# Optimization experiments

Measured on AMD Instinct MI355X. Metric: run time of the kernel, lower is better.

Reference implementation:

```python
import jax, jax.numpy as jnp
import numpy as np
import math

B, D, H, N, L = 32, 64, 8, 4096, 12
DK = D // H  # 8
APT = 10

def conv1x1_relu(x, w, b):
    # x: [B, C, N, L]; w: [O, C]; b: [O]  (1x1 conv == channel matmul)
    return jax.nn.relu(jnp.einsum('oc,bcnl->bonl', w, x) + b[None, :, None, None])

def setup_inputs() -> dict:
    key = jax.random.key(0)
    ks = jax.random.split(key, 12)
    s = 1.0 / math.sqrt(D)
    return {
        'x': jax.random.normal(ks[0], (B, D, N, L), jnp.float32),
        'wq': jax.random.normal(ks[1], (D, D), jnp.float32) * s,
        'bq': jnp.zeros((D,), jnp.float32),
        'wv': jax.random.normal(ks[2], (D, D), jnp.float32) * s,
        'bv': jnp.zeros((D,), jnp.float32),
        'wc': jax.random.normal(ks[3], (D, D), jnp.float32) * s,
        'bc': jnp.zeros((D,), jnp.float32),
        'memory': jax.random.normal(ks[4], (H, L, N, DK), jnp.float32) * 0.02,
        'weight': jnp.ones((D, N, L), jnp.float32),
        'bias': jnp.zeros((D, N, L), jnp.float32),
        'nv1': jax.random.normal(ks[5], (N, APT), jnp.float32),
        'nv2': jax.random.normal(ks[6], (APT, N), jnp.float32),
    }

def reference(x, wq, bq, wv, bv, wc, bc, memory, weight, bias, nv1, nv2):
    scale = 1.0 / math.sqrt(DK)
    q = conv1x1_relu(x, wq, bq)               # [B, D, N, L]
    v = conv1x1_relu(x, wv, bv)               # [B, D, N, L]
    # [B, D, N, L] -> [B, H, dk, N, L] -> [B, H, L, N, dk]
    v5 = jnp.transpose(v.reshape(B, H, DK, N, L), (0, 1, 4, 3, 2))
    q5 = jnp.transpose(q.reshape(B, H, DK, N, L), (0, 1, 4, 3, 2))
    key_sm = jax.nn.softmax(memory * scale, axis=-1)       # [H, L, N, dk]
    q_sm = jax.nn.softmax(q5 * scale, axis=-1)             # [B, H, L, N, dk]
    Aapt = jax.nn.softmax(jax.nn.relu(nv1 @ nv2), axis=-1) # [N, N]
    kv = jnp.einsum('hlnx,bhlny->bhlxy', key_sm, v5)       # [B,H,L,dk,dk]
    attn_qkv = jnp.einsum('bhlnx,bhlxy->bhlny', q_sm, kv)  # [B,H,L,N,dk]
    # 'nm,bhlnc->bhlnc' sums Aapt over m -> row-sum scaling of value
    row = jnp.sum(Aapt, axis=1)                            # [N]
    attn_dyn = row[None, None, None, :, None] * v5
    y = attn_qkv + attn_dyn                                # [B,H,L,N,dk]
    y = jnp.transpose(y, (0, 1, 4, 3, 2)).reshape(B, D, N, L)
    y = conv1x1_relu(y, wc, bc)
    out = y * weight[None] + bias[None] + y
    return out
```

## Files before the change

kernel.cpp:

```cpp
#include <hip/hip_runtime.h>
#include <math.h>
#include <stdint.h>

#define BB 32
#define DD 64
#define HH 8
#define NNN 4096
#define LL 12
#define PP (NNN * LL)

#define NTILES_A 24
#define CHUNK_A (64 * NTILES_A)
#define NCHUNK_A (PP / CHUNK_A)

#define NTILES_B 12
#define CHUNK_B (64 * NTILES_B)
#define NCHUNK_B (PP / CHUNK_B)

#define VSTRIDE 68
#define SCALE 0.35355339059327373f

typedef const __attribute__((address_space(1))) uint32_t gu32;
typedef __attribute__((address_space(3))) uint32_t lu32;

__device__ __forceinline__ void dma16(const float* src, float* dst) {
    __builtin_amdgcn_global_load_lds((gu32*)src, (lu32*)dst, 16, 0, 0);
}

__device__ __forceinline__ int xsw(int p, int c4) {
    return (p << 6) + (((c4 ^ (p & 7)) & 15) << 2);
}

__global__ void prep(const float* __restrict__ wq, const float* __restrict__ wv,
                     const float* __restrict__ wc, float* __restrict__ wt)
{
    const int i = blockIdx.x * 256 + threadIdx.x;
    const int o = i >> 6, c = i & 63;
    wt[c * 64 + o]        = wq[i];
    wt[4096 + c * 64 + o] = wv[i];
    wt[8192 + c * 64 + o] = wc[i];
}

__global__ void prep_ksm(const float* __restrict__ mem, float* __restrict__ ksm)
{
    const int g = blockIdx.x * 256 + threadIdx.x;
    const int p = g >> 3, h = g & 7;
    const int n = p / 12, l = p - n * 12;
    const float4* mp = (const float4*)(mem + (((size_t)(h * 12 + l) * NNN + n) << 3));
    float4 a0 = mp[0], a1 = mp[1];
    float v0 = a0.x * SCALE, v1 = a0.y * SCALE, v2 = a0.z * SCALE, v3 = a0.w * SCALE;
    float v4 = a1.x * SCALE, v5 = a1.y * SCALE, v6 = a1.z * SCALE, v7 = a1.w * SCALE;
    float m = fmaxf(fmaxf(fmaxf(v0, v1), fmaxf(v2, v3)),
                    fmaxf(fmaxf(v4, v5), fmaxf(v6, v7)));
    float e0 = __expf(v0 - m), e1 = __expf(v1 - m), e2 = __expf(v2 - m), e3 = __expf(v3 - m);
    float e4 = __expf(v4 - m), e5 = __expf(v5 - m), e6 = __expf(v6 - m), e7 = __expf(v7 - m);
    float inv = 1.0f / (e0 + e1 + e2 + e3 + e4 + e5 + e6 + e7);
    float4* op = (float4*)(ksm + ((size_t)g << 3));
    op[0] = make_float4(e0 * inv, e1 * inv, e2 * inv, e3 * inv);
    op[1] = make_float4(e4 * inv, e5 * inv, e6 * inv, e7 * inv);
}

__global__ void prep_wb(const float* __restrict__ wgt, const float* __restrict__ bsa,
                        float* __restrict__ wb)
{
    const size_t i = (size_t)blockIdx.x * 256 + threadIdx.x;
    wb[i * 2]     = wgt[i] + 1.0f;
    wb[i * 2 + 1] = bsa[i];
}

__global__ __launch_bounds__(512, 2)
void pass_a(const float* __restrict__ x, const float* __restrict__ wvt,
            const float* __restrict__ bv, const float* __restrict__ mem,
            const float* __restrict__ ksm,
            float* __restrict__ kv)
{
    __shared__ float xb0[64 * 64];
    __shared__ float xb1[64 * 64];
    __shared__ float ksl[64 * 64];
    __shared__ float v_tile[64 * VSTRIDE];

    const int t = threadIdx.x;
    const int b = blockIdx.y;
    const int chunk0 = blockIdx.x * CHUNK_A;

    const int p1 = t & 63;
    const int og = t >> 6;
    const int o0 = og << 3;
    const int o0u = __builtin_amdgcn_readfirstlane(o0);
    const float* __restrict__ wvu = wvt + o0u;

    float bvl[8];
#pragma unroll
    for (int j = 0; j < 8; j++) bvl[j] = bv[o0 + j];

    const int wid = t >> 6;
    const int ln  = t & 63;
    const int g_r = ln >> 4;
    const int g_c4 = (ln & 15) << 2;

    const int h2 = (t >> 3) & 7;
    const int x2 = t & 7;
    const int l0 = t >> 6;
    const int l1 = 8 + (t >> 6);
    const bool has2 = (t < 256);

    float acc[2][8];
#pragma unroll
    for (int q = 0; q < 2; q++)
#pragma unroll
        for (int y = 0; y < 8; y++) acc[q][y] = 0.f;

    const float* xb = x + (size_t)(b * 64) * PP;

    auto issue_x = [&](float* dst, int pn) {
        const int r0 = wid << 3;
        dma16(xb + (size_t)(r0 + g_r) * PP + pn + g_c4, dst + (r0 << 6));
        dma16(xb + (size_t)(r0 + 4 + g_r) * PP + pn + g_c4, dst + ((r0 + 4) << 6));
    };
    auto issue_ks = [&](int pn) {
        const int fo = wid << 9;
        const float* s0 = ksm + (((size_t)pn) << 6) + fo + (ln << 2);
        dma16(s0, ksl + fo);
        dma16(s0 + 256, ksl + fo + 256);
    };
    auto fallback_ks = [&](int pbase) {
        int pos = t >> 3, h = t & 7;
        int pg = pbase + pos;
        int n = pg / 12;
        int l = pg - n * 12;
        const float4* mp = (const float4*)(mem + (((size_t)(h * 12 + l) * NNN + n) << 3));
        float4 a0 = mp[0], a1 = mp[1];
        float v0 = a0.x * SCALE, v1 = a0.y * SCALE, v2 = a0.z * SCALE, v3 = a0.w * SCALE;
        float v4 = a1.x * SCALE, v5 = a1.y * SCALE, v6 = a1.z * SCALE, v7 = a1.w * SCALE;
        float m = fmaxf(fmaxf(fmaxf(v0, v1), fmaxf(v2, v3)),
                        fmaxf(fmaxf(v4, v5), fmaxf(v6, v7)));
        float e0 = __expf(v0 - m), e1 = __expf(v1 - m), e2 = __expf(v2 - m), e3 = __expf(v3 - m);
        float e4 = __expf(v4 - m), e5 = __expf(v5 - m), e6 = __expf(v6 - m), e7 = __expf(v7 - m);
        float inv = 1.0f / (e0 + e1 + e2 + e3 + e4 + e5 + e6 + e7);
        float4* kp = (float4*)(ksl + (pos << 6) + (h << 3));
        kp[0] = make_float4(e0 * inv, e1 * inv, e2 * inv, e3 * inv);
        kp[1] = make_float4(e4 * inv, e5 * inv, e6 * inv, e7 * inv);
    };

    issue_x(xb0, chunk0);
    if (ksm) issue_ks(chunk0); else fallback_ks(chunk0);
    __syncthreads();

    for (int tile = 0; tile < NTILES_A; tile++) {
        const int pbase = chunk0 + tile * 64;
        float* bufA = (tile & 1) ? xb1 : xb0;
        float* bufB = (tile & 1) ? xb0 : xb1;
        const bool more = (tile + 1) < NTILES_A;

        if (more) issue_x(bufB, pbase + 64);

        float va[8];
#pragma unroll
        for (int j = 0; j < 8; j++) va[j] = 0.f;
        for (int c = 0; c < 64; c += 4) {
            float xs0 = bufA[(c << 6) + p1];
            float xs1 = bufA[((c + 1) << 6) + p1];
            float xs2 = bufA[((c + 2) << 6) + p1];
            float xs3 = bufA[((c + 3) << 6) + p1];
            const float* w0 = wvu + c * 64;
#pragma unroll
            for (int j = 0; j < 8; j++) {
                va[j] += w0[j] * xs0;
                va[j] += w0[64 + j] * xs1;
                va[j] += w0[128 + j] * xs2;
                va[j] += w0[192 + j] * xs3;
            }
        }
        {
            const int slot = ((og ^ (p1 >> 3)) & 7) << 3;
            float4* vt4 = (float4*)(v_tile + p1 * VSTRIDE + slot);
            float4 w;
            w.x = fmaxf(va[0] + bvl[0], 0.f);
            w.y = fmaxf(va[1] + bvl[1], 0.f);
            w.z = fmaxf(va[2] + bvl[2], 0.f);
            w.w = fmaxf(va[3] + bvl[3], 0.f);
            vt4[0] = w;
            w.x = fmaxf(va[4] + bvl[4], 0.f);
            w.y = fmaxf(va[5] + bvl[5], 0.f);
            w.z = fmaxf(va[6] + bvl[6], 0.f);
            w.w = fmaxf(va[7] + bvl[7], 0.f);
            vt4[1] = w;
        }
        __syncthreads();

        const int r = pbase % 12;
        {
            int s = l0 - r;
            if (s < 0) s += 12;
            for (int p = s; p < 64; p += 12) {
                float ksv = ksl[(p << 6) + (h2 << 3) + x2];
                const int slot = ((h2 ^ (p >> 3)) & 7) << 3;
                const float4* vp = (const float4*)(v_tile + p * VSTRIDE + slot);
                float4 u0 = vp[0], u1 = vp[1];
                acc[0][0] += ksv * u0.x; acc[0][1] += ksv * u0.y;
                acc[0][2] += ksv * u0.z; acc[0][3] += ksv * u0.w;
                acc[0][4] += ksv * u1.x; acc[0][5] += ksv * u1.y;
                acc[0][6] += ksv * u1.z; acc[0][7] += ksv * u1.w;
            }
        }
        if (has2) {
            int s = l1 - r;
            if (s < 0) s += 12;
            for (int p = s; p < 64; p += 12) {
                float ksv = ksl[(p << 6) + (h2 << 3) + x2];
                const int slot = ((h2 ^ (p >> 3)) & 7) << 3;
                const float4* vp = (const float4*)(v_tile + p * VSTRIDE + slot);
                float4 u0 = vp[0], u1 = vp[1];
                acc[1][0] += ksv * u0.x; acc[1][1] += ksv * u0.y;
                acc[1][2] += ksv * u0.z; acc[1][3] += ksv * u0.w;
                acc[1][4] += ksv * u1.x; acc[1][5] += ksv * u1.y;
                acc[1][6] += ksv * u1.z; acc[1][7] += ksv * u1.w;
            }
        }
        __syncthreads();

        if (more) { if (ksm) issue_ks(pbase + 64); else fallback_ks(pbase + 64); }
    }

    {
        float* kvp = kv + (((size_t)((b * 12 + l0) * 8 + h2)) << 6) + (x2 << 3);
#pragma unroll
        for (int y = 0; y < 8; y++) atomicAdd(kvp + y, acc[0][y]);
    }
    if (has2) {
        float* kvp = kv + (((size_t)((b * 12 + l1) * 8 + h2)) << 6) + (x2 << 3);
#pragma unroll
        for (int y = 0; y < 8; y++) atomicAdd(kvp + y, acc[1][y]);
    }
}

__global__ __launch_bounds__(256, 2)
void pass_b(const float* __restrict__ x, const float* __restrict__ wqt,
            const float* __restrict__ wvt, const float* __restrict__ wct,
            const float* __restrict__ bq, const float* __restrict__ bv,
            const float* __restrict__ bc, const float* __restrict__ kv,
            const float* __restrict__ wgt, const float* __restrict__ bsa,
            const float* __restrict__ wb,
            float* __restrict__ out)
{
    __shared__ float xt[64 * 64];
    __shared__ float yt[64 * 64];
    __shared__ float kv_lds[12 * 512];

    const int t = threadIdx.x;
    const int b = blockIdx.y;
    const int chunk0 = blockIdx.x * CHUNK_B;

    const int p1 = t & 63;
    const int og = t >> 6;
    const int o0 = og << 4;
    const int o0u = __builtin_amdgcn_readfirstlane(o0);
    const float* __restrict__ wqu = wqt + o0u;
    const float* __restrict__ wvu = wvt + o0u;
    const float* __restrict__ wcu = wct + o0u;

    const int sx_c  = t >> 4;
    const int sx_p4 = (t & 15) << 2;

    float bql[16], bvl[16], bcl[16];
#pragma unroll
    for (int j = 0; j < 16; j++) {
        bql[j] = bq[o0 + j];
        bvl[j] = bv[o0 + j];
        bcl[j] = bc[o0 + j];
    }

    const float* xb = x + (size_t)(b * 64) * PP;
    float* ob = out + (size_t)(b * 64) * PP;

    {
        const float* kvb = kv + (size_t)b * 6144;
        for (int i = t; i < 6144; i += 256) {
            const int l = i >> 9;
            const int h = (i >> 6) & 7;
            const int xx = (i >> 3) & 7;
            const int y = i & 7;
            kv_lds[(l << 9) + (h << 6) + ((xx ^ (l & 3)) << 3) + y] = kvb[i];
        }
#pragma unroll
        for (int r = 0; r < 4; r++) {
            const int c = r * 16 + sx_c;
            float4 a = *(const float4*)(xb + (size_t)c * PP + chunk0 + sx_p4);
            xt[xsw(sx_p4 + 0, c >> 2) + (c & 3)] = a.x;
            xt[xsw(sx_p4 + 1, c >> 2) + (c & 3)] = a.y;
            xt[xsw(sx_p4 + 2, c >> 2) + (c & 3)] = a.z;
            xt[xsw(sx_p4 + 3, c >> 2) + (c & 3)] = a.w;
        }
    }
    __syncthreads();

    for (int tile_i = 0; tile_i < NTILES_B; tile_i++) {
        const int pbase = chunk0 + tile_i * 64;
        const int pg = pbase + p1;
        const int l = pg % 12;
        const bool more = (tile_i + 1) < NTILES_B;

        float qa[16], va[16];
#pragma unroll
        for (int j = 0; j < 16; j++) { qa[j] = 0.f; va[j] = 0.f; }
        for (int c = 0; c < 64; c += 4) {
            const float4 xv = *(const float4*)(xt + xsw(p1, c >> 2));
            const float* q0 = wqu + c * 64;
            const float* v0 = wvu + c * 64;
#pragma unroll
            for (int j = 0; j < 16; j++) {
                qa[j] += q0[j] * xv.x;       va[j] += v0[j] * xv.x;
                qa[j] += q0[64 + j] * xv.y;  va[j] += v0[64 + j] * xv.y;
                qa[j] += q0[128 + j] * xv.z; va[j] += v0[128 + j] * xv.z;
                qa[j] += q0[192 + j] * xv.w; va[j] += v0[192 + j] * xv.w;
            }
        }
#pragma unroll
        for (int j = 0; j < 16; j++) {
            qa[j] = fmaxf(qa[j] + bql[j], 0.f) * SCALE;
            va[j] = fmaxf(va[j] + bvl[j], 0.f);
        }

#pragma unroll
        for (int hh = 0; hh < 2; hh++) {
            float* qh = qa + hh * 8;
            float m = fmaxf(fmaxf(fmaxf(qh[0], qh[1]), fmaxf(qh[2], qh[3])),
                            fmaxf(fmaxf(qh[4], qh[5]), fmaxf(qh[6], qh[7])));
            float s = 0.f;
#pragma unroll
            for (int xk = 0; xk < 8; xk++) { qh[xk] = __expf(qh[xk] - m); s += qh[xk]; }
            float inv = 1.0f / s;
#pragma unroll
            for (int xk = 0; xk < 8; xk++) qh[xk] *= inv;
        }

        const int lsw = l & 3;
        float yv[2][8];
#pragma unroll
        for (int hh = 0; hh < 2; hh++) {
            const int h = og * 2 + hh;
            const float* kvp = kv_lds + (l << 9) + (h << 6);
#pragma unroll
            for (int y = 0; y < 8; y++) yv[hh][y] = va[hh * 8 + y];
#pragma unroll
            for (int xk = 0; xk < 8; xk++) {
                float qv = qa[hh * 8 + xk];
                const float4* kp = (const float4*)(kvp + ((xk ^ lsw) << 3));
                float4 k0 = kp[0], k1 = kp[1];
                yv[hh][0] += qv * k0.x; yv[hh][1] += qv * k0.y;
                yv[hh][2] += qv * k0.z; yv[hh][3] += qv * k0.w;
                yv[hh][4] += qv * k1.x; yv[hh][5] += qv * k1.y;
                yv[hh][6] += qv * k1.z; yv[hh][7] += qv * k1.w;
            }
        }
        {
            const int oq = og << 2;
            *(float4*)(yt + xsw(p1, oq + 0)) = make_float4(yv[0][0], yv[0][1], yv[0][2], yv[0][3]);
            *(float4*)(yt + xsw(p1, oq + 1)) = make_float4(yv[0][4], yv[0][5], yv[0][6], yv[0][7]);
            *(float4*)(yt + xsw(p1, oq + 2)) = make_float4(yv[1][0], yv[1][1], yv[1][2], yv[1][3]);
            *(float4*)(yt + xsw(p1, oq + 3)) = make_float4(yv[1][4], yv[1][5], yv[1][6], yv[1][7]);
        }
        __syncthreads();

        float4 st0, st1, st2, st3;
        if (more) {
            const int pn = pbase + 64;
            st0 = *(const float4*)(xb + (size_t)(sx_c) * PP + pn + sx_p4);
            st1 = *(const float4*)(xb + (size_t)(sx_c + 16) * PP + pn + sx_p4);
            st2 = *(const float4*)(xb + (size_t)(sx_c + 32) * PP + pn + sx_p4);
            st3 = *(const float4*)(xb + (size_t)(sx_c + 48) * PP + pn + sx_p4);
        }

        float ca[16];
#pragma unroll
        for (int j = 0; j < 16; j++) ca[j] = 0.f;
        for (int c = 0; c < 64; c += 4) {
            const float4 yv4 = *(const float4*)(yt + xsw(p1, c >> 2));
            const float* w0 = wcu + c * 64;
#pragma unroll
            for (int j = 0; j < 16; j++) {
                ca[j] += w0[j] * yv4.x;
                ca[j] += w0[64 + j] * yv4.y;
                ca[j] += w0[128 + j] * yv4.z;
                ca[j] += w0[192 + j] * yv4.w;
            }
        }
        if (wb) {
#pragma unroll
            for (int j = 0; j < 16; j++) {
                float yc = fmaxf(ca[j] + bcl[j], 0.f);
                size_t oi = (size_t)(o0 + j) * PP + pg;
                float2 w2 = *(const float2*)(wb + oi * 2);
                ob[oi] = yc * w2.x + w2.y;
            }
        } else {
#pragma unroll
            for (int j = 0; j < 16; j++) {
                float yc = fmaxf(ca[j] + bcl[j], 0.f);
                size_t oi = (size_t)(o0 + j) * PP + pg;
                ob[oi] = yc * (wgt[oi] + 1.0f) + bsa[oi];
            }
        }

        if (more) {
            const int c0 = sx_c, c1 = sx_c + 16, c2 = sx_c + 32, c3 = sx_c + 48;
            xt[xsw(sx_p4 + 0, c0 >> 2) + (c0 & 3)] = st0.x;
            xt[xsw(sx_p4 + 1, c0 >> 2) + (c0 & 3)] = st0.y;
            xt[xsw(sx_p4 + 2, c0 >> 2) + (c0 & 3)] = st0.z;
            xt[xsw(sx_p4 + 3, c0 >> 2) + (c0 & 3)] = st0.w;
            xt[xsw(sx_p4 + 0, c1 >> 2) + (c1 & 3)] = st1.x;
            xt[xsw(sx_p4 + 1, c1 >> 2) + (c1 & 3)] = st1.y;
            xt[xsw(sx_p4 + 2, c1 >> 2) + (c1 & 3)] = st1.z;
            xt[xsw(sx_p4 + 3, c1 >> 2) + (c1 & 3)] = st1.w;
            xt[xsw(sx_p4 + 0, c2 >> 2) + (c2 & 3)] = st2.x;
            xt[xsw(sx_p4 + 1, c2 >> 2) + (c2 & 3)] = st2.y;
            xt[xsw(sx_p4 + 2, c2 >> 2) + (c2 & 3)] = st2.z;
            xt[xsw(sx_p4 + 3, c2 >> 2) + (c2 & 3)] = st2.w;
            xt[xsw(sx_p4 + 0, c3 >> 2) + (c3 & 3)] = st3.x;
            xt[xsw(sx_p4 + 1, c3 >> 2) + (c3 & 3)] = st3.y;
            xt[xsw(sx_p4 + 2, c3 >> 2) + (c3 & 3)] = st3.z;
            xt[xsw(sx_p4 + 3, c3 >> 2) + (c3 & 3)] = st3.w;
        }
        __syncthreads();
    }
}

extern "C" void kernel_launch(void* const* d_in, const int* in_sizes, int n_in,
                              void* d_out, int out_size, void* d_ws, size_t ws_size,
                              hipStream_t stream) {
    const float* x   = (const float*)d_in[0];
    const float* wq  = (const float*)d_in[1];
    const float* bq  = (const float*)d_in[2];
    const float* wv  = (const float*)d_in[3];
    const float* bv  = (const float*)d_in[4];
    const float* wc  = (const float*)d_in[5];
    const float* bc  = (const float*)d_in[6];
    const float* mem = (const float*)d_in[7];
    const float* wgt = (const float*)d_in[8];
    const float* bsa = (const float*)d_in[9];
    float* outp = (float*)d_out;

    const size_t kv_floats  = (size_t)BB * LL * HH * 64;
    const size_t wt_floats  = 3 * 4096;
    const size_t ksm_floats = (size_t)PP * 64;
    const size_t wb_floats  = (size_t)PP * 64 * 2;

    float* kvw = (float*)d_ws;
    float* wt  = kvw + kv_floats;
    float* ksm = wt + wt_floats;
    float* wb  = ksm + ksm_floats;
    const bool have_ksm =
        ws_size >= (kv_floats + wt_floats + ksm_floats) * sizeof(float);
    const bool have_wb =
        ws_size >= (kv_floats + wt_floats + ksm_floats + wb_floats) * sizeof(float);

    hipMemsetAsync(kvw, 0, kv_floats * sizeof(float), stream);

    prep<<<16, 256, 0, stream>>>(wq, wv, wc, wt);
    if (have_ksm) {
        prep_ksm<<<(PP * 8) / 256, 256, 0, stream>>>(mem, ksm);
    }
    if (have_wb) {
        prep_wb<<<(PP * 64) / 256, 256, 0, stream>>>(wgt, bsa, wb);
    }

    dim3 grid_a(NCHUNK_A, BB);
    pass_a<<<grid_a, 512, 0, stream>>>(x, wt + 4096, bv, mem,
                                       have_ksm ? ksm : nullptr, kvw);
    dim3 grid_b(NCHUNK_B, BB);
    pass_b<<<grid_b, 256, 0, stream>>>(x, wt, wt + 4096, wt + 8192,
                                       bq, bv, bc, kvw, wgt, bsa,
                                       have_wb ? wb : nullptr, outp);
}
```

Baseline: 1.590 ms.

## Double pass_b threads to 512, halve per-thread output channels, raise occupancy bounds

pass_b now runs 512 threads per block. Each wave handles 8 output channels (one head) instead of 16, which roughly halves the accumulator register arrays. Biases are folded into the accumulator initialisation, and launch bounds on both passes ask for 4 blocks per CU, while the pass_b chunk is doubled to 24 tiles. The aim is lower register pressure and higher occupancy to hide memory latency, at the cost of more redundant weight and LDS reads per output and fewer blocks in the grid.

New measurement: 1.782 ms. +12.1%, slower.

```diff
diff --git a/kernel.cpp b/kernel.cpp
--- a/kernel.cpp
+++ b/kernel.cpp
@@ -13,7 +13,7 @@
 #define CHUNK_A (64 * NTILES_A)
 #define NCHUNK_A (PP / CHUNK_A)
 
-#define NTILES_B 12
+#define NTILES_B 24
 #define CHUNK_B (64 * NTILES_B)
 #define NCHUNK_B (PP / CHUNK_B)
 
@@ -68,7 +68,7 @@
     wb[i * 2 + 1] = bsa[i];
 }
 
-__global__ __launch_bounds__(512, 2)
+__global__ __launch_bounds__(512, 4)
 void pass_a(const float* __restrict__ x, const float* __restrict__ wvt,
             const float* __restrict__ bv, const float* __restrict__ mem,
             const float* __restrict__ ksm,
@@ -91,7 +91,7 @@
 
     float bvl[8];
 #pragma unroll
-    for (int j = 0; j < 8; j++) bvl[j] = bv[o0 + j];
+    for (int j = 0; j < 8; j++) bvl[j] = bv[o0u + j];
 
     const int wid = t >> 6;
     const int ln  = t & 63;
@@ -234,7 +234,7 @@
     }
 }
 
-__global__ __launch_bounds__(256, 2)
+__global__ __launch_bounds__(512, 4)
 void pass_b(const float* __restrict__ x, const float* __restrict__ wqt,
             const float* __restrict__ wvt, const float* __restrict__ wct,
             const float* __restrict__ bq, const float* __restrict__ bv,
@@ -253,44 +253,47 @@
 
     const int p1 = t & 63;
     const int og = t >> 6;
-    const int o0 = og << 4;
+    const int o0 = og << 3;
     const int o0u = __builtin_amdgcn_readfirstlane(o0);
     const float* __restrict__ wqu = wqt + o0u;
     const float* __restrict__ wvu = wvt + o0u;
     const float* __restrict__ wcu = wct + o0u;
 
+    float bql[8], bvl[8], bcl[8];
+#pragma unroll
+    for (int j = 0; j < 8; j++) {
+        bql[j] = bq[o0u + j];
+        bvl[j] = bv[o0u + j];
+        bcl[j] = bc[o0u + j];
+    }
+
     const int sx_c  = t >> 4;
     const int sx_p4 = (t & 15) << 2;
 
-    float bql[16], bvl[16], bcl[16];
-#pragma unroll
-    for (int j = 0; j < 16; j++) {
-        bql[j] = bq[o0 + j];
-        bvl[j] = bv[o0 + j];
-        bcl[j] = bc[o0 + j];
-    }
-
     const float* xb = x + (size_t)(b * 64) * PP;
     float* ob = out + (size_t)(b * 64) * PP;
 
     {
         const float* kvb = kv + (size_t)b * 6144;
-        for (int i = t; i < 6144; i += 256) {
+        for (int i = t; i < 6144; i += 512) {
             const int l = i >> 9;
             const int h = (i >> 6) & 7;
             const int xx = (i >> 3) & 7;
             const int y = i & 7;
             kv_lds[(l << 9) + (h << 6) + ((xx ^ (l & 3)) << 3) + y] = kvb[i];
         }
-#pragma unroll
-        for (int r = 0; r < 4; r++) {
-            const int c = r * 16 + sx_c;
-            float4 a = *(const float4*)(xb + (size_t)c * PP + chunk0 + sx_p4);
-            xt[xsw(sx_p4 + 0, c >> 2) + (c & 3)] = a.x;
-            xt[xsw(sx_p4 + 1, c >> 2) + (c & 3)] = a.y;
-            xt[xsw(sx_p4 + 2, c >> 2) + (c & 3)] = a.z;
-            xt[xsw(sx_p4 + 3, c >> 2) + (c & 3)] = a.w;
-        }
+        float4 a0 = *(const float4*)(xb + (size_t)sx_c * PP + chunk0 + sx_p4);
+        float4 a1 = *(const float4*)(xb + (size_t)(sx_c + 32) * PP + chunk0 + sx_p4);
+        const int c4a = sx_c >> 2, ra = sx_c & 3;
+        const int c4b = c4a + 8,   rb = ra;
+        xt[xsw(sx_p4 + 0, c4a) + ra] = a0.x;
+        xt[xsw(sx_p4 + 1, c4a) + ra] = a0.y;
+        xt[xsw(sx_p4 + 2, c4a) + ra] = a0.z;
+        xt[xsw(sx_p4 + 3, c4a) + ra] = a0.w;
+        xt[xsw(sx_p4 + 0, c4b) + rb] = a1.x;
+        xt[xsw(sx_p4 + 1, c4b) + rb] = a1.y;
+        xt[xsw(sx_p4 + 2, c4b) + rb] = a1.z;
+        xt[xsw(sx_p4 + 3, c4b) + rb] = a1.w;
     }
     __syncthreads();
 
@@ -300,15 +303,15 @@
         const int l = pg % 12;
         const bool more = (tile_i + 1) < NTILES_B;
 
-        float qa[16], va[16];
-#pragma unroll
-        for (int j = 0; j < 16; j++) { qa[j] = 0.f; va[j] = 0.f; }
+        float qa[8], va[8];
+#pragma unroll
+        for (int j = 0; j < 8; j++) { qa[j] = bql[j]; va[j] = bvl[j]; }
         for (int c = 0; c < 64; c += 4) {
             const float4 xv = *(const float4*)(xt + xsw(p1, c >> 2));
             const float* q0 = wqu + c * 64;
             const float* v0 = wvu + c * 64;
 #pragma unroll
-            for (int j = 0; j < 16; j++) {
+            for (int j = 0; j < 8; j++) {
                 qa[j] += q0[j] * xv.x;       va[j] += v0[j] * xv.x;
                 qa[j] += q0[64 + j] * xv.y;  va[j] += v0[64 + j] * xv.y;
                 qa[j] += q0[128 + j] * xv.z; va[j] += v0[128 + j] * xv.z;
@@ -316,69 +319,61 @@
             }
         }
 #pragma unroll
-        for (int j = 0; j < 16; j++) {
-            qa[j] = fmaxf(qa[j] + bql[j], 0.f) * SCALE;
-            va[j] = fmaxf(va[j] + bvl[j], 0.f);
-        }
-
-#pragma unroll
-        for (int hh = 0; hh < 2; hh++) {
-            float* qh = qa + hh * 8;
-            float m = fmaxf(fmaxf(fmaxf(qh[0], qh[1]), fmaxf(qh[2], qh[3])),
-                            fmaxf(fmaxf(qh[4], qh[5]), fmaxf(qh[6], qh[7])));
+        for (int j = 0; j < 8; j++) {
+            qa[j] = fmaxf(qa[j], 0.f) * SCALE;
+            va[j] = fmaxf(va[j], 0.f);
+        }
+
+        {
+            float m = fmaxf(fmaxf(fmaxf(qa[0], qa[1]), fmaxf(qa[2], qa[3])),
+                            fmaxf(fmaxf(qa[4], qa[5]), fmaxf(qa[6], qa[7])));
             float s = 0.f;
 #pragma unroll
-            for (int xk = 0; xk < 8; xk++) { qh[xk] = __expf(qh[xk] - m); s += qh[xk]; }
+            for (int xk = 0; xk < 8; xk++) { qa[xk] = __expf(qa[xk] - m); s += qa[xk]; }
             float inv = 1.0f / s;
 #pragma unroll
-            for (int xk = 0; xk < 8; xk++) qh[xk] *= inv;
+            for (int xk = 0; xk < 8; xk++) qa[xk] *= inv;
         }
 
         const int lsw = l & 3;
-        float yv[2][8];
-#pragma unroll
-        for (int hh = 0; hh < 2; hh++) {
-            const int h = og * 2 + hh;
-            const float* kvp = kv_lds + (l << 9) + (h << 6);
-#pragma unroll
-            for (int y = 0; y < 8; y++) yv[hh][y] = va[hh * 8 + y];
+        float yv[8];
+#pragma unroll
+        for (int y = 0; y < 8; y++) yv[y] = va[y];
+        {
+            const float* kvp = kv_lds + (l << 9) + (og << 6);
 #pragma unroll
             for (int xk = 0; xk < 8; xk++) {
-                float qv = qa[hh * 8 + xk];
+                float qv = qa[xk];
                 const float4* kp = (const float4*)(kvp + ((xk ^ lsw) << 3));
                 float4 k0 = kp[0], k1 = kp[1];
-                yv[hh][0] += qv * k0.x; yv[hh][1] += qv * k0.y;
-                yv[hh][2] += qv * k0.z; yv[hh][3] += qv * k0.w;
-                yv[hh][4] += qv * k1.x; yv[hh][5] += qv * k1.y;
-                yv[hh][6] += qv * k1.z; yv[hh][7] += qv * k1.w;
+                yv[0] += qv * k0.x; yv[1] += qv * k0.y;
+                yv[2] += qv * k0.z; yv[3] += qv * k0.w;
+                yv[4] += qv * k1.x; yv[5] += qv * k1.y;
+                yv[6] += qv * k1.z; yv[7] += qv * k1.w;
             }
         }
         {
-            const int oq = og << 2;
-            *(float4*)(yt + xsw(p1, oq + 0)) = make_float4(yv[0][0], yv[0][1], yv[0][2], yv[0][3]);
-            *(float4*)(yt + xsw(p1, oq + 1)) = make_float4(yv[0][4], yv[0][5], yv[0][6], yv[0][7]);
-            *(float4*)(yt + xsw(p1, oq + 2)) = make_float4(yv[1][0], yv[1][1], yv[1][2], yv[1][3]);
-            *(float4*)(yt + xsw(p1, oq + 3)) = make_float4(yv[1][4], yv[1][5], yv[1][6], yv[1][7]);
+            const int oq = og << 1;
+            *(float4*)(yt + xsw(p1, oq + 0)) = make_float4(yv[0], yv[1], yv[2], yv[3]);
+            *(float4*)(yt + xsw(p1, oq + 1)) = make_float4(yv[4], yv[5], yv[6], yv[7]);
         }
         __syncthreads();
 
-        float4 st0, st1, st2, st3;
+        float4 st0, st1;
         if (more) {
             const int pn = pbase + 64;
-            st0 = *(const float4*)(xb + (size_t)(sx_c) * PP + pn + sx_p4);
-            st1 = *(const float4*)(xb + (size_t)(sx_c + 16) * PP + pn + sx_p4);
-            st2 = *(const float4*)(xb + (size_t)(sx_c + 32) * PP + pn + sx_p4);
-            st3 = *(const float4*)(xb + (size_t)(sx_c + 48) * PP + pn + sx_p4);
-        }
-
-        float ca[16];
-#pragma unroll
-        for (int j = 0; j < 16; j++) ca[j] = 0.f;
+            st0 = *(const float4*)(xb + (size_t)sx_c * PP + pn + sx_p4);
+            st1 = *(const float4*)(xb + (size_t)(sx_c + 32) * PP + pn + sx_p4);
+        }
+
+        float ca[8];
+#pragma unroll
+        for (int j = 0; j < 8; j++) ca[j] = bcl[j];
         for (int c = 0; c < 64; c += 4) {
             const float4 yv4 = *(const float4*)(yt + xsw(p1, c >> 2));
             const float* w0 = wcu + c * 64;
 #pragma unroll
-            for (int j = 0; j < 16; j++) {
+            for (int j = 0; j < 8; j++) {
                 ca[j] += w0[j] * yv4.x;
                 ca[j] += w0[64 + j] * yv4.y;
                 ca[j] += w0[128 + j] * yv4.z;
@@ -387,39 +382,32 @@
         }
         if (wb) {
 #pragma unroll
-            for (int j = 0; j < 16; j++) {
-                float yc = fmaxf(ca[j] + bcl[j], 0.f);
+            for (int j = 0; j < 8; j++) {
+                float yc = fmaxf(ca[j], 0.f);
                 size_t oi = (size_t)(o0 + j) * PP + pg;
                 float2 w2 = *(const float2*)(wb + oi * 2);
                 ob[oi] = yc * w2.x + w2.y;
             }
         } else {
 #pragma unroll
-            for (int j = 0; j < 16; j++) {
-                float yc = fmaxf(ca[j] + bcl[j], 0.f);
+            for (int j = 0; j < 8; j++) {
+                float yc = fmaxf(ca[j], 0.f);
                 size_t oi = (size_t)(o0 + j) * PP + pg;
                 ob[oi] = yc * (wgt[oi] + 1.0f) + bsa[oi];
             }
         }
 
         if (more) {
-            const int c0 = sx_c, c1 = sx_c + 16, c2 = sx_c + 32, c3 = sx_c + 48;
-            xt[xsw(sx_p4 + 0, c0 >> 2) + (c0 & 3)] = st0.x;
-            xt[xsw(sx_p4 + 1, c0 >> 2) + (c0 & 3)] = st0.y;
-            xt[xsw(sx_p4 + 2, c0 >> 2) + (c0 & 3)] = st0.z;
-            xt[xsw(sx_p4 + 3, c0 >> 2) + (c0 & 3)] = st0.w;
-            xt[xsw(sx_p4 + 0, c1 >> 2) + (c1 & 3)] = st1.x;
-            xt[xsw(sx_p4 + 1, c1 >> 2) + (c1 & 3)] = st1.y;
-            xt[xsw(sx_p4 + 2, c1 >> 2) + (c1 & 3)] = st1.z;
-            xt[xsw(sx_p4 + 3, c1 >> 2) + (c1 & 3)] = st1.w;
-            xt[xsw(sx_p4 + 0, c2 >> 2) + (c2 & 3)] = st2.x;
-            xt[xsw(sx_p4 + 1, c2 >> 2) + (c2 & 3)] = st2.y;
-            xt[xsw(sx_p4 + 2, c2 >> 2) + (c2 & 3)] = st2.z;
-            xt[xsw(sx_p4 + 3, c2 >> 2) + (c2 & 3)] = st2.w;
-            xt[xsw(sx_p4 + 0, c3 >> 2) + (c3 & 3)] = st3.x;
-            xt[xsw(sx_p4 + 1, c3 >> 2) + (c3 & 3)] = st3.y;
-            xt[xsw(sx_p4 + 2, c3 >> 2) + (c3 & 3)] = st3.z;
-            xt[xsw(sx_p4 + 3, c3 >> 2) + (c3 & 3)] = st3.w;
+            const int c4a = sx_c >> 2, ra = sx_c & 3;
+            const int c4b = c4a + 8,   rb = ra;
+            xt[xsw(sx_p4 + 0, c4a) + ra] = st0.x;
+            xt[xsw(sx_p4 + 1, c4a) + ra] = st0.y;
+            xt[xsw(sx_p4 + 2, c4a) + ra] = st0.z;
+            xt[xsw(sx_p4 + 3, c4a) + ra] = st0.w;
+            xt[xsw(sx_p4 + 0, c4b) + rb] = st1.x;
+            xt[xsw(sx_p4 + 1, c4b) + rb] = st1.y;
+            xt[xsw(sx_p4 + 2, c4b) + rb] = st1.z;
+            xt[xsw(sx_p4 + 3, c4b) + rb] = st1.w;
         }
         __syncthreads();
     }
@@ -468,7 +456,7 @@
     pass_a<<<grid_a, 512, 0, stream>>>(x, wt + 4096, bv, mem,
                                        have_ksm ? ksm : nullptr, kvw);
     dim3 grid_b(NCHUNK_B, BB);
-    pass_b<<<grid_b, 256, 0, stream>>>(x, wt, wt + 4096, wt + 8192,
+    pass_b<<<grid_b, 512, 0, stream>>>(x, wt, wt + 4096, wt + 8192,
                                        bq, bv, bc, kvw, wgt, bsa,
                                        have_wb ? wb : nullptr, outp);
 }
```
